# Optimization experiments

Hardware: AMD Instinct MI355X
Metric: run time of the kernel (lower is better)

Reference implementation:

```python
import jax, jax.numpy as jnp
import numpy as np

BN_EPS = 1e-5

def conv1x1(x, w, b):
    # x: [N,C,T,V], w: [O,C], b: [O]
    return jnp.einsum('nctv,oc->notv', x, w) + b[None, :, None, None]

def conv9(x, w, b):
    # (9,1) temporal conv, padding (4,0). x: [N,C,T,V], w: [O,C,9], b: [O]
    out = jax.lax.conv_general_dilated(
        x, w[:, :, :, None], window_strides=(1, 1), padding=((4, 4), (0, 0)),
        dimension_numbers=('NCHW', 'OIHW', 'NCHW'))
    return out + b[None, :, None, None]

def attn_adj(f1, f2):
    # f1,f2: [N,inter,T,V] -> softmax over rows (axis -2) of [N,V,V]
    N, ic, T, V = f1.shape
    a1 = jnp.transpose(f1, (0, 3, 1, 2)).reshape(N, V, ic * T)  # permute(0,3,1,2).view
    a2 = f2.reshape(N, ic * T, V)
    scores = jnp.einsum('nvk,nkw->nvw', a1, a2) / (ic * T)
    return jax.nn.softmax(scores, axis=-2)


def setup_inputs() -> dict:
    key = jax.random.key(0)
    ks = jax.random.split(key, 16)
    N, C, T, V, S, IC = 16, 256, 64, 25, 3, 64
    s = lambda k, shape, sc=0.05: jax.random.normal(k, shape, dtype=jnp.float32) * sc
    return {
        'x': jax.random.normal(ks[0], (N, C, T, V), dtype=jnp.float32),
        'A': jax.random.uniform(ks[1], (S, V, V), dtype=jnp.float32),
        'PA': s(ks[2], (S, V, V), 1e-3),
        'wa': s(ks[3], (S, IC, C)), 'ba': jnp.zeros((S, IC), jnp.float32),
        'wb': s(ks[4], (S, IC, C)), 'bb': jnp.zeros((S, IC), jnp.float32),
        'wT1': s(ks[5], (S, IC, C, 9)), 'bT1': jnp.zeros((S, IC), jnp.float32),
        'wT2': s(ks[6], (S, IC, C, 9)), 'bT2': jnp.zeros((S, IC), jnp.float32),
        'wST11': s(ks[7], (S, IC, C, 9)), 'bST11': jnp.zeros((S, IC), jnp.float32),
        'wST12': s(ks[8], (S, IC, C, 9)), 'bST12': jnp.zeros((S, IC), jnp.float32),
        'wd': s(ks[9], (S, C, C)), 'bd': jnp.zeros((S, C), jnp.float32),
        'gamma': jnp.ones((C,), jnp.float32), 'beta': jnp.zeros((C,), jnp.float32),
        'bn_mean': jnp.zeros((C,), jnp.float32), 'bn_var': jnp.ones((C,), jnp.float32),
    }


def reference(x, A, PA, wa, ba, wb, bb, wT1, bT1, wT2, bT2,
              wST11, bST11, wST12, bST12, wd, bd, gamma, beta, bn_mean, bn_var):
    N, C, T, V = x.shape
    I = jnp.eye(V, dtype=x.dtype)
    # Chebyshev-like static graph transforms (computed once in __init__ in torch)
    A_ch4s = jax.nn.softmax((8 * A**4 - 4 * A**2 - 4 * A + I) / V, axis=-2)
    A_ch3 = 4 * A**2 - A - 2 * I
    A_all = A_ch3 + A_ch4s + PA  # [3,V,V]

    xf = x.reshape(N, C * T, V)
    y = 0.0
    for i in range(3):
        A1 = attn_adj(conv1x1(x, wa[i], ba[i]), conv1x1(x, wb[i], bb[i]))
        AT = attn_adj(conv9(x, wT1[i], bT1[i]), conv9(x, wT2[i], bT2[i]))
        # ModuleList append quirk: even i -> 1x1 conv (center tap), odd i -> (9,1) conv
        if i % 2 == 0:
            s1 = conv1x1(x, wST11[i, :, :, 4], bST11[i])
            s2 = conv1x1(x, wST12[i, :, :, 4], bST12[i])
        else:
            s1 = conv9(x, wST11[i], bST11[i])
            s2 = conv9(x, wST12[i], bST12[i])
        AST = attn_adj(s1, s2)
        Ai = A_all[i] + A1 + AT + AST  # [N,V,V]
        z = jnp.einsum('nkv,nvw->nkw', xf, Ai).reshape(N, C, T, V)
        y = y + conv1x1(z, wd[i], bd[i])

    yb = (y - bn_mean[None, :, None, None]) * (gamma[None, :, None, None]
         / jnp.sqrt(bn_var[None, :, None, None] + BN_EPS)) + beta[None, :, None, None]
    return jax.nn.relu(yb + x)  # down is identity (in_channels == out_channels)
```

## Files before the change

### kernel.cpp

```cpp
#include <hip/hip_runtime.h>
#include <hip/hip_bf16.h>

#define NN 16
#define CC 256
#define TT 64
#define VV 25
#define ICC 64
#define TV 1600
#define CTV 409600
#define NICTV 1638400

typedef __bf16 v8bf __attribute__((ext_vector_type(8)));
typedef __bf16 v4bf __attribute__((ext_vector_type(4)));
typedef float f32x16 __attribute__((ext_vector_type(16)));

struct ConvPairs {
  const __bf16* wA[5];
  const __bf16* wB[5];
  const float*  bA[5];
  const float*  bB[5];
};

__device__ __forceinline__ void gl_lds16(const __bf16* g, __bf16* l){
  __builtin_amdgcn_global_load_lds(
      (const __attribute__((address_space(1))) unsigned int*)g,
      (__attribute__((address_space(3))) unsigned int*)l, 16, 0, 0);
}

__global__ __launch_bounds__(256) void prep_k(
    const float* __restrict__ x, __bf16* __restrict__ xt,
    const float* __restrict__ wT1, const float* __restrict__ wT2,
    const float* __restrict__ wST11, const float* __restrict__ wST12,
    __bf16* __restrict__ wT1p, __bf16* __restrict__ wT2p,
    __bf16* __restrict__ wS1p, __bf16* __restrict__ wS2p,
    const float* __restrict__ wa, const float* __restrict__ wb,
    __bf16* __restrict__ wabp, __bf16* __restrict__ wScp,
    const float* __restrict__ wd, __bf16* __restrict__ wdb,
    const float* __restrict__ A, const float* __restrict__ PA,
    float* __restrict__ Aall, __bf16* __restrict__ zp){
  __shared__ __align__(16) float smf[64*65];
  __bf16* smb = (__bf16*)smf;
  int b = blockIdx.x;
  int tid = threadIdx.x;
  if (b < 64){
    int t = b >> 3, ch64 = (b >> 1) & 3, o2 = b & 1;
    const float* src; __bf16* dst;
    if (t < 3)      { src = wT1  + (size_t)t*147456;     dst = wT1p + (size_t)t*147456; }
    else if (t < 6) { src = wT2  + (size_t)(t-3)*147456; dst = wT2p + (size_t)(t-3)*147456; }
    else if (t == 6){ src = wST11 + 147456;              dst = wS1p; }
    else            { src = wST12 + 147456;              dst = wS2p; }
    const float* in = src + (size_t)(o2*32)*2304 + ch64*576;
    for (int i = tid; i < 32*576; i += 256){
      int row = i / 576, cc = i % 576;
      smb[i] = (__bf16)in[(size_t)row*2304 + cc];
    }
    __syncthreads();
    for (int i = tid; i < 18432; i += 256){
      int e = i & 7, l = (i >> 3) & 63, ks = (i >> 9) & 1;
      int r10 = i >> 10;
      int tap = r10 % 9, chh = r10 / 9;
      int ol = l & 31, hh = l >> 5;
      int cl = ks*16 + hh*8 + e;
      int c64 = chh*32 + cl;
      int ch8 = ch64*2 + chh;
      dst[(size_t)((((ch8*9 + tap)*2 + ks)*2 + o2)*512) + l*8 + e]
          = smb[ol*576 + c64*9 + tap];
    }
  } else if (b < 74){
    int u = b - 64;
    for (int it = 0; it < 8; ++it){
      int i = tid + it*256;
      int e = i & 7, l = (i >> 3) & 63, o2 = (i >> 9) & 1;
      int ks = (i >> 10) & 1, ch = i >> 11;
      int ol = l & 31, hh = l >> 5;
      int o = o2*32 + ol;
      int c = ch*32 + ks*16 + hh*8 + e;
      __bf16 v;
      if (u < 6){
        const float* w = (u < 3) ? (wa + (size_t)u*16384) : (wb + (size_t)(u-3)*16384);
        v = (__bf16)w[(size_t)o*256 + c];
      } else {
        int i9 = ((u == 6) || (u == 8)) ? 0 : 2;
        const float* w = ((u < 8) ? wST11 : wST12) + (size_t)i9*147456;
        v = (__bf16)w[((size_t)o*256 + c)*9 + 4];
      }
      __bf16* dst = (u < 6) ? (wabp + (size_t)u*16384) : (wScp + (size_t)(u-6)*16384);
      dst[i] = v;
    }
  } else if (b < 842){
    int i = (b-74)*256 + tid;
    if (i < 196608) wdb[i] = (__bf16)wd[i];
  } else if (b == 842){
    int t = tid;
    if (t < 75){
      int s = t / 25, w = t % 25;
      float a[25], m[25];
      float mx = -3.4e38f;
      for (int v = 0; v < 25; ++v){
        float av = A[(s*25 + v)*25 + w];
        a[v] = av;
        float d = (v == w) ? 1.f : 0.f;
        float mm = (8.f*av*av*av*av - 4.f*av*av - 4.f*av + d) * 0.04f;
        m[v] = mm;
        mx = fmaxf(mx, mm);
      }
      float sum = 0.f;
      for (int v = 0; v < 25; ++v){ float e = __expf(m[v]-mx); m[v] = e; sum += e; }
      float inv = 1.f/sum;
      for (int v = 0; v < 25; ++v){
        float av = a[v];
        float d = (v == w) ? 1.f : 0.f;
        Aall[(s*25+v)*25 + w] = m[v]*inv + 4.f*av*av - av - 2.f*d + PA[(s*25+v)*25+w];
      }
    } else if (t >= 128){
      zp[t-128] = (__bf16)0.f;
    }
  } else {
    int idx = b - 843;
    int p0 = (idx % 25)*64, c0 = ((idx/25) & 3)*64, n = idx/100;
    for (int i = tid; i < 4096; i += 256){
      int cc = i >> 6, pp = i & 63;
      smf[cc*65+pp] = x[(size_t)n*CTV + (size_t)(c0+cc)*TV + p0 + pp];
    }
    __syncthreads();
    for (int i = tid; i < 4096; i += 256){
      int pp = i >> 6, cc = i & 63;
      xt[((size_t)n*TV + p0+pp)*256 + c0+cc] = (__bf16)smf[cc*65+pp];
    }
  }
}

template<int NTAPS>
__global__ __launch_bounds__(512, 4) void conv14_k(const __bf16* __restrict__ xt,
    ConvPairs cp, const __bf16* __restrict__ zp, __bf16* __restrict__ fbuf){
  extern __shared__ __bf16 sm[];
  constexpr int HALO  = (NTAPS==9) ? 100 : 0;
  constexpr int NROWS = 256 + 2*HALO;
  constexpr int SLOTS = NROWS*4;
  constexpr int KSTG  = (SLOTS + 511)/512;
  constexpr int NSTEP = NTAPS*2;
  int p0 = blockIdx.x*256;
  int n  = blockIdx.y;
  int pr = blockIdx.z;
  int tid = threadIdx.x;
  int lane = tid & 63;
  int wave = tid >> 6;
  int which = wave >> 2, wq = wave & 3;
  int h = lane >> 5, l31 = lane & 31;
  const __bf16* wp = (which ? cp.wB[pr] : cp.wA[pr]) + lane*8;
  const __bf16* xtn = xt + (size_t)n*CTV;
  __bf16* buf0 = sm;
  __bf16* buf1 = sm + NROWS*32;

  f32x16 acc[2][2];
  #pragma unroll
  for (int a=0;a<2;++a)
    #pragma unroll
    for (int b=0;b<2;++b)
      #pragma unroll
      for (int r=0;r<16;++r) acc[a][b][r] = 0.f;

  int rowbase = wq*64 + l31;

  auto stage = [&](__bf16* bn, int ch){
    #pragma unroll
    for (int k=0; k<KSTG; ++k){
      int slot = k*512 + tid;
      if ((SLOTS & 511) && slot >= SLOTS) continue;
      const __bf16* src;
      if (NTAPS == 1){
        int l31s = slot & 31, f = slot >> 5;
        int h_ = f & 1, ks_ = (f >> 1) & 1, pblk = f >> 2;
        int pg = p0 + pblk*32 + l31s;
        src = (pg < 1600) ? (xtn + (size_t)pg*256 + ch*32 + ks_*16 + h_*8)
                          : zp;
      } else {
        int row = slot >> 2, g2 = slot & 3;
        int g = (g2 - (row>>1)) & 3;
        int pg = p0 - HALO + row;
        src = ((unsigned)pg < 1600u) ? (xtn + (size_t)pg*256 + ch*32 + g*8)
                                     : zp;
      }
      gl_lds16(src, bn + (size_t)slot*8);
    }
  };
  auto ldA = [&](int ch, int s, v8bf* aa){
    int tap = s >> 1, ks = s & 1;
    size_t o = (size_t)(((ch*NTAPS + tap)*2 + ks)*2)*512;
    aa[0] = *(const v8bf*)(wp + o);
    aa[1] = *(const v8bf*)(wp + o + 512);
  };
  auto ldB = [&](const __bf16* bc, int s, v8bf* bb){
    int tap = s >> 1, ks = s & 1;
    #pragma unroll
    for (int pq=0; pq<2; ++pq){
      if (NTAPS == 1){
        int frag = ((wq*2 + pq)*2 + ks)*2 + h;
        bb[pq] = *(const v8bf*)(bc + frag*256 + l31*8);
      } else {
        int row = tap*25 + rowbase + pq*32;
        int gs = ((ks*2 + h) + (row>>1)) & 3;
        bb[pq] = *(const v8bf*)(bc + row*32 + gs*8);
      }
    }
  };

  v8bf ar[2][2];
  ldA(0, 0, ar[0]);
  ldA(0, 1, ar[1]);
  stage(buf0, 0);
  __syncthreads();

  for (int ch=0; ch<8; ++ch){
    const __bf16* bc = (ch & 1) ? buf1 : buf0;
    __bf16*       bn = (ch & 1) ? buf0 : buf1;
    if (ch < 7) stage(bn, ch+1);
    v8bf bR[2][2];
    ldB(bc, 0, bR[0]);
    if (NSTEP > 1) ldB(bc, 1, bR[1]);
    #pragma unroll
    for (int s=0; s<NSTEP; ++s){
      int c = s & 1;
      v8bf A0 = ar[c][0], A1 = ar[c][1];
      v8bf B0 = bR[c][0], B1 = bR[c][1];
      if (s+2 < NSTEP){
        ldB(bc, s+2, bR[c]);
        ldA(ch, s+2, ar[c]);
      } else if (ch < 7){
        ldA(ch+1, s+2-NSTEP, ar[c]);
      }
      acc[0][0] = __builtin_amdgcn_mfma_f32_32x32x16_bf16(A0, B0, acc[0][0], 0,0,0);
      acc[1][0] = __builtin_amdgcn_mfma_f32_32x32x16_bf16(A1, B0, acc[1][0], 0,0,0);
      acc[0][1] = __builtin_amdgcn_mfma_f32_32x32x16_bf16(A0, B1, acc[0][1], 0,0,0);
      acc[1][1] = __builtin_amdgcn_mfma_f32_32x32x16_bf16(A1, B1, acc[1][1], 0,0,0);
    }
    __syncthreads();
  }

  const float* bias = which ? cp.bB[pr] : cp.bA[pr];
  __bf16* outb = fbuf + (size_t)(pr*2 + which)*NICTV + (size_t)n*TV*64;
  #pragma unroll
  for (int pq=0; pq<2; ++pq){
    int p = p0 + wq*64 + pq*32 + l31;
    if (p >= 1600) continue;
    __bf16* orow = outb + (size_t)p*64;
    #pragma unroll
    for (int of=0; of<2; ++of){
      #pragma unroll
      for (int g=0; g<4; ++g){
        int og = of*32 + 8*g + 4*h;
        v4bf pk;
        #pragma unroll
        for (int j=0;j<4;++j) pk[j] = (__bf16)(acc[of][pq][4*g+j] + bias[og+j]);
        *(v4bf*)(orow + og) = pk;
      }
    }
  }
}

__global__ __launch_bounds__(256, 2) void ugemm6_k(const __bf16* __restrict__ xt,
    const __bf16* __restrict__ wdb, __bf16* __restrict__ ubuf){
  __shared__ __bf16 sm[64*256];
  int p0 = blockIdx.x*64;
  int n  = blockIdx.y;
  int tid = threadIdx.x;
  int lane = tid & 63;
  int os = tid >> 6;
  int h = lane >> 5, l31 = lane & 31;
  const __bf16* xtn = xt + (size_t)n*CTV;

  for (int s2 = tid; s2 < 64*32; s2 += 256){
    int row = s2 >> 5, g = s2 & 31;
    uint4 val = *(const uint4*)(xtn + (size_t)(p0+row)*256 + g*8);
    int gs = (g + row) & 31;
    *(uint4*)(sm + row*256 + gs*8) = val;
  }
  __syncthreads();

  auto ldB = [&](int ks, v8bf* bb){
    #pragma unroll
    for (int pq=0; pq<2; ++pq){
      int row = pq*32 + l31;
      int gs = ((ks*2 + h) + row) & 31;
      bb[pq] = *(const v8bf*)(sm + row*256 + gs*8);
    }
  };

  for (int br=0; br<3; ++br){
    const __bf16* wl = wdb + ((size_t)br*256 + os*64 + l31)*256 + h*8;
    auto ldA = [&](int ks, v8bf& A0, v8bf& A1){
      A0 = *(const v8bf*)(wl + ks*16);
      A1 = *(const v8bf*)(wl + (size_t)32*256 + ks*16);
    };
    f32x16 acc[2][2];
    #pragma unroll
    for (int a=0;a<2;++a)
      #pragma unroll
      for (int b=0;b<2;++b)
        #pragma unroll
        for (int r=0;r<16;++r) acc[a][b][r] = 0.f;

    v8bf a0[4], a1[4];
    ldA(0, a0[0], a1[0]);
    ldA(1, a0[1], a1[1]);
    ldA(2, a0[2], a1[2]);
    ldA(3, a0[3], a1[3]);
    v8bf bR[2][2];
    ldB(0, bR[0]);
    ldB(1, bR[1]);
    #pragma unroll
    for (int ks=0; ks<16; ++ks){
      int c2 = ks & 1, cur = ks & 3;
      v8bf B0 = bR[c2][0], B1 = bR[c2][1];
      v8bf A0 = a0[cur], A1 = a1[cur];
      if (ks+2 < 16) ldB(ks+2, bR[c2]);
      if (ks+4 < 16) ldA(ks+4, a0[cur], a1[cur]);
      acc[0][0] = __builtin_amdgcn_mfma_f32_32x32x16_bf16(A0, B0, acc[0][0], 0,0,0);
      acc[1][0] = __builtin_amdgcn_mfma_f32_32x32x16_bf16(A1, B0, acc[1][0], 0,0,0);
      acc[0][1] = __builtin_amdgcn_mfma_f32_32x32x16_bf16(A0, B1, acc[0][1], 0,0,0);
      acc[1][1] = __builtin_amdgcn_mfma_f32_32x32x16_bf16(A1, B1, acc[1][1], 0,0,0);
    }

    #pragma unroll
    for (int pq=0; pq<2; ++pq){
      int p = p0 + pq*32 + l31;
      __bf16* out = ubuf + ((size_t)(br*NN + n)*TV + p)*256;
      #pragma unroll
      for (int oq=0; oq<2; ++oq){
        #pragma unroll
        for (int g=0; g<4; ++g){
          int og = os*64 + oq*32 + 8*g + 4*h;
          v4bf pk;
          #pragma unroll
          for (int j=0;j<4;++j) pk[j] = (__bf16)acc[oq][pq][4*g+j];
          *(v4bf*)(out + og) = pk;
        }
      }
    }
  }
}

__global__ __launch_bounds__(256) void scores_m_k(const __bf16* __restrict__ fbuf,
                                                  float* __restrict__ part, int pairbase){
  int n = blockIdx.y, pr = blockIdx.z;
  int tid = threadIdx.x;
  int lane = tid & 63;
  int wave = tid >> 6;
  int chunk = blockIdx.x*4 + wave;
  int h = lane >> 5, l31 = lane & 31;
  const __bf16* f1 = fbuf + (size_t)(pr*2)*NICTV   + (size_t)n*TV*64;
  const __bf16* f2 = fbuf + (size_t)(pr*2+1)*NICTV + (size_t)n*TV*64;
  int t0 = chunk*4;

  f32x16 acc;
  #pragma unroll
  for (int r=0;r<16;++r) acc[r] = 0.f;

  auto off = [&](int s)->size_t{
    int t = t0 + (s>>2), og = s&3;
    return ((size_t)(t*25 + l31))*64 + og*16 + h*8;
  };
  v8bf A[4], B[4];
  #pragma unroll
  for (int i=0; i<4; ++i){
    size_t o = off(i);
    A[i] = *(const v8bf*)(f1+o); B[i] = *(const v8bf*)(f2+o);
  }
  #pragma unroll
  for (int s=0; s<16; ++s){
    int cur = s & 3;
    v8bf Ac = A[cur], Bc = B[cur];
    if (s+4 < 16){
      size_t o2 = off(s+4);
      A[cur] = *(const v8bf*)(f1+o2);
      B[cur] = *(const v8bf*)(f2+o2);
    }
    acc = __builtin_amdgcn_mfma_f32_32x32x16_bf16(Ac, Bc, acc, 0,0,0);
  }

  size_t tile = (((size_t)(pairbase+pr)*NN + n)*16 + chunk);
  float* pt = part + tile*1024;
  #pragma unroll
  for (int r=0; r<16; ++r){
    int row = (r&3) + 8*(r>>2) + 4*h;
    pt[row*32 + l31] = acc[r];
  }
}

__global__ __launch_bounds__(64) void reduce_all_k(const float* __restrict__ part,
    const float* __restrict__ Aall, float* __restrict__ Ai3){
  const int pairbr[9] = {0,1,2,0,2, 0,1,2,1};
  int n = blockIdx.x, w = blockIdx.y;
  int lane = threadIdx.x;
  float accbr[3] = {0.f, 0.f, 0.f};
  for (int pr=0; pr<9; ++pr){
    float s = 0.f;
    if (lane < 25){
      const float* pp = part + (((size_t)pr*NN + n)*16)*1024 + lane*32 + w;
      #pragma unroll
      for (int ch=0; ch<16; ++ch) s += pp[(size_t)ch*1024];
    }
    s *= (1.f/4096.f);
    float mval = (lane<25) ? s : -3.4e38f;
    #pragma unroll
    for (int d=32; d>0; d>>=1) mval = fmaxf(mval, __shfl_xor(mval, d));
    float e = (lane<25) ? __expf(s - mval) : 0.f;
    float sum = e;
    #pragma unroll
    for (int d=32; d>0; d>>=1) sum += __shfl_xor(sum, d);
    accbr[pairbr[pr]] += e / sum;
  }
  if (lane < 25){
    #pragma unroll
    for (int br=0; br<3; ++br)
      Ai3[((size_t)br*NN + n)*625 + lane*25 + w] =
        Aall[br*625 + lane*25 + w] + accbr[br];
  }
}

__global__ __launch_bounds__(256) void yep_k(const float* __restrict__ x,
    const float* __restrict__ Ai3, const __bf16* __restrict__ ubuf,
    const float* __restrict__ bd, const float* __restrict__ gamma,
    const float* __restrict__ beta, const float* __restrict__ bnm,
    const float* __restrict__ bnv, float* __restrict__ out){
  __shared__ float ais[3][25*28];
  int t = blockIdx.x, n = blockIdx.y, o = threadIdx.x;
  for (int l=o; l<2100; l+=256){
    int br = l/700, r = l%700;
    int v = r/28, w = r%28;
    ais[br][v*28+w] = (w<25) ? Ai3[((size_t)br*NN + n)*625 + v*25 + w] : 0.f;
  }
  __syncthreads();
  float y[28];
  #pragma unroll
  for (int w=0;w<28;++w) y[w]=0.f;
  for (int br=0; br<3; ++br){
    const __bf16* up = ubuf + ((size_t)(br*NN + n)*TV + t*25)*256 + o;
    float uv[25];
    #pragma unroll
    for (int v=0;v<25;++v) uv[v] = (float)up[(size_t)v*256];
    const float* ab = ais[br];
    for (int v=0; v<25; ++v){
      float u = uv[v];
      #pragma unroll
      for (int j=0; j<7; ++j){
        float4 a4 = *(const float4*)(ab + v*28 + 4*j);
        y[4*j+0] = fmaf(u, a4.x, y[4*j+0]);
        y[4*j+1] = fmaf(u, a4.y, y[4*j+1]);
        y[4*j+2] = fmaf(u, a4.z, y[4*j+2]);
        y[4*j+3] = fmaf(u, a4.w, y[4*j+3]);
      }
    }
  }
  float bsum = bd[o] + bd[256+o] + bd[512+o];
  float sc = gamma[o] * rsqrtf(bnv[o] + 1e-5f);
  float m  = bnm[o], be = beta[o];
  const float* xr = x + (size_t)n*CTV + (size_t)o*TV + t*25;
  float* orow = out + (size_t)n*CTV + (size_t)o*TV + t*25;
  #pragma unroll
  for (int w=0; w<25; ++w)
    orow[w] = fmaxf((y[w] + bsum - m)*sc + be + xr[w], 0.f);
}

extern "C" void kernel_launch(void* const* d_in, const int* in_sizes, int n_in,
                              void* d_out, int out_size, void* d_ws, size_t ws_size,
                              hipStream_t stream) {
  const float* x     = (const float*)d_in[0];
  const float* A     = (const float*)d_in[1];
  const float* PA    = (const float*)d_in[2];
  const float* wa    = (const float*)d_in[3];
  const float* ba    = (const float*)d_in[4];
  const float* wb    = (const float*)d_in[5];
  const float* bb    = (const float*)d_in[6];
  const float* wT1   = (const float*)d_in[7];
  const float* bT1   = (const float*)d_in[8];
  const float* wT2   = (const float*)d_in[9];
  const float* bT2   = (const float*)d_in[10];
  const float* wST11 = (const float*)d_in[11];
  const float* bST11 = (const float*)d_in[12];
  const float* wST12 = (const float*)d_in[13];
  const float* bST12 = (const float*)d_in[14];
  const float* wd    = (const float*)d_in[15];
  const float* bd    = (const float*)d_in[16];
  const float* gamma = (const float*)d_in[17];
  const float* beta  = (const float*)d_in[18];
  const float* bnm   = (const float*)d_in[19];
  const float* bnv   = (const float*)d_in[20];

  char* W = (char*)d_ws;
  float*  Aall = (float*)W;  W += 8192;
  __bf16* zp   = (__bf16*)W; W += 256;
  float*  Ai3  = (float*)W;  W += 122880;
  __bf16* wabp = (__bf16*)W; W += 196608;
  __bf16* wScp = (__bf16*)W; W += 131072;
  __bf16* wT1p = (__bf16*)W; W += 884736;
  __bf16* wT2p = (__bf16*)W; W += 884736;
  __bf16* wS1p = (__bf16*)W; W += 294912;
  __bf16* wS2p = (__bf16*)W; W += 294912;
  __bf16* wdb  = (__bf16*)W; W += 393216;
  __bf16* xt   = (__bf16*)W; W += 13107200;
  char* R = W;               W += 39321600;
  float*  part = (float*)W;  W += 9437184;
  __bf16* fbuf = (__bf16*)R;
  __bf16* ubuf = (__bf16*)R;

  prep_k<<<2443, 256, 0, stream>>>(x, xt, wT1, wT2, wST11, wST12,
                                   wT1p, wT2p, wS1p, wS2p,
                                   wa, wb, wabp, wScp, wd, wdb, A, PA, Aall, zp);

  {
    ConvPairs cp;
    for (int i=0;i<3;++i){
      cp.wA[i] = wabp + (size_t)i*16384;      cp.wB[i] = wabp + (size_t)(3+i)*16384;
      cp.bA[i] = ba + i*64;                   cp.bB[i] = bb + i*64;
    }
    int evens[2] = {0, 2};
    for (int j=0;j<2;++j){
      int i = evens[j];
      cp.wA[3+j] = wScp + (size_t)j*16384;    cp.wB[3+j] = wScp + (size_t)(2+j)*16384;
      cp.bA[3+j] = bST11 + i*64;              cp.bB[3+j] = bST12 + i*64;
    }
    conv14_k<1><<<dim3(7,16,5), 512, 2*256*32*2, stream>>>(xt, cp, zp, fbuf);
    scores_m_k<<<dim3(4,16,5), 256, 0, stream>>>(fbuf, part, 0);
  }

  {
    ConvPairs cp;
    for (int i=0;i<3;++i){
      cp.wA[i] = wT1p + (size_t)i*147456;  cp.wB[i] = wT2p + (size_t)i*147456;
      cp.bA[i] = bT1 + i*64;               cp.bB[i] = bT2 + i*64;
    }
    cp.wA[3] = wS1p;  cp.wB[3] = wS2p;
    cp.bA[3] = bST11 + 64;  cp.bB[3] = bST12 + 64;
    cp.wA[4] = cp.wA[3]; cp.wB[4] = cp.wB[3]; cp.bA[4] = cp.bA[3]; cp.bB[4] = cp.bB[3];
    conv14_k<9><<<dim3(7,16,4), 512, 2*456*32*2, stream>>>(xt, cp, zp, fbuf);
    scores_m_k<<<dim3(4,16,4), 256, 0, stream>>>(fbuf, part, 5);
  }

  ugemm6_k<<<dim3(25,16), 256, 0, stream>>>(xt, wdb, ubuf);
  reduce_all_k<<<dim3(16,25), 64, 0, stream>>>(part, Aall, Ai3);
  yep_k<<<dim3(64,16), 256, 0, stream>>>(x, Ai3, ubuf, bd, gamma, beta, bnm, bnv,
                                         (float*)d_out);
}
```

Before: 338.4 us.

## Stage conv weights through LDS and deepen MFMA operand prefetch

The conv kernel now copies each channel chunk's weight slices for both conv branches into shared memory with async global-to-LDS loads, instead of having every wave read weights directly from global memory. Operand prefetch depth for the 9-tap variant goes from 2 to 3, and MFMA issue is wrapped in s_setprio. The goal is to cut redundant global weight traffic and hide load latency. In exchange, the 9-tap kernel uses far more shared memory (about 132 KB), which lowers occupancy (min waves per EU reduced to 2), and it adds an extra barrier per chunk because weight staging is not double-buffered.

```diff
diff --git a/kernel.cpp b/kernel.cpp
--- a/kernel.cpp
+++ b/kernel.cpp
@@ -130,8 +130,8 @@
   }
 }
 
-template<int NTAPS>
-__global__ __launch_bounds__(512, 4) void conv14_k(const __bf16* __restrict__ xt,
+template<int NTAPS, int MINW>
+__global__ __launch_bounds__(512, MINW) void conv15_k(const __bf16* __restrict__ xt,
     ConvPairs cp, const __bf16* __restrict__ zp, __bf16* __restrict__ fbuf){
   extern __shared__ __bf16 sm[];
   constexpr int HALO  = (NTAPS==9) ? 100 : 0;
@@ -139,6 +139,9 @@
   constexpr int SLOTS = NROWS*4;
   constexpr int KSTG  = (SLOTS + 511)/512;
   constexpr int NSTEP = NTAPS*2;
+  constexpr int AELE  = NTAPS*2*2*512;
+  constexpr int ASLT  = 2*AELE/8;
+  constexpr int DEP   = (NSTEP >= 3) ? 3 : 2;
   int p0 = blockIdx.x*256;
   int n  = blockIdx.y;
   int pr = blockIdx.z;
@@ -147,10 +150,12 @@
   int wave = tid >> 6;
   int which = wave >> 2, wq = wave & 3;
   int h = lane >> 5, l31 = lane & 31;
-  const __bf16* wp = (which ? cp.wB[pr] : cp.wA[pr]) + lane*8;
   const __bf16* xtn = xt + (size_t)n*CTV;
-  __bf16* buf0 = sm;
-  __bf16* buf1 = sm + NROWS*32;
+  const __bf16* wg0 = cp.wA[pr];
+  const __bf16* wg1 = cp.wB[pr];
+  __bf16* xb0 = sm;
+  __bf16* xb1 = sm + NROWS*32;
+  __bf16* Ab  = sm + 2*NROWS*32;
 
   f32x16 acc[2][2];
   #pragma unroll
@@ -162,7 +167,7 @@
 
   int rowbase = wq*64 + l31;
 
-  auto stage = [&](__bf16* bn, int ch){
+  auto stageX = [&](__bf16* bn, int ch){
     #pragma unroll
     for (int k=0; k<KSTG; ++k){
       int slot = k*512 + tid;
@@ -184,11 +189,22 @@
       gl_lds16(src, bn + (size_t)slot*8);
     }
   };
-  auto ldA = [&](int ch, int s, v8bf* aa){
-    int tap = s >> 1, ks = s & 1;
-    size_t o = (size_t)(((ch*NTAPS + tap)*2 + ks)*2)*512;
-    aa[0] = *(const v8bf*)(wp + o);
-    aa[1] = *(const v8bf*)(wp + o + 512);
+  auto stageA = [&](int ch){
+    #pragma unroll
+    for (int k=0; k<(ASLT+511)/512; ++k){
+      int slot = k*512 + tid;
+      if ((ASLT & 511) && slot >= ASLT) continue;
+      int cv = (slot >= AELE/8) ? 1 : 0;
+      int off = (slot - cv*(AELE/8))*8;
+      const __bf16* src = (cv ? wg1 : wg0) + (size_t)ch*AELE + off;
+      gl_lds16(src, Ab + cv*AELE + off);
+    }
+  };
+  const __bf16* aw = Ab + which*AELE + lane*8;
+  auto ldA = [&](int s, v8bf* aa){
+    int off = s*1024;
+    aa[0] = *(const v8bf*)(aw + off);
+    aa[1] = *(const v8bf*)(aw + off + 512);
   };
   auto ldB = [&](const __bf16* bc, int s, v8bf* bb){
     int tap = s >> 1, ks = s & 1;
@@ -205,35 +221,37 @@
     }
   };
 
-  v8bf ar[2][2];
-  ldA(0, 0, ar[0]);
-  ldA(0, 1, ar[1]);
-  stage(buf0, 0);
+  stageA(0);
+  stageX(xb0, 0);
   __syncthreads();
 
+  v8bf ar[DEP][2], bR[DEP][2];
   for (int ch=0; ch<8; ++ch){
-    const __bf16* bc = (ch & 1) ? buf1 : buf0;
-    __bf16*       bn = (ch & 1) ? buf0 : buf1;
-    if (ch < 7) stage(bn, ch+1);
-    v8bf bR[2][2];
-    ldB(bc, 0, bR[0]);
-    if (NSTEP > 1) ldB(bc, 1, bR[1]);
+    const __bf16* bc = (ch & 1) ? xb1 : xb0;
+    __bf16*       bn = (ch & 1) ? xb0 : xb1;
+    if (ch < 7) stageX(bn, ch+1);
+    #pragma unroll
+    for (int i=0; i<DEP; ++i){
+      if (i < NSTEP){ ldA(i, ar[i]); ldB(bc, i, bR[i]); }
+    }
     #pragma unroll
     for (int s=0; s<NSTEP; ++s){
-      int c = s & 1;
+      int c = s % DEP;
       v8bf A0 = ar[c][0], A1 = ar[c][1];
       v8bf B0 = bR[c][0], B1 = bR[c][1];
-      if (s+2 < NSTEP){
-        ldB(bc, s+2, bR[c]);
-        ldA(ch, s+2, ar[c]);
-      } else if (ch < 7){
-        ldA(ch+1, s+2-NSTEP, ar[c]);
-      }
+      if (s+DEP < NSTEP){
+        ldB(bc, s+DEP, bR[c]);
+        ldA(s+DEP, ar[c]);
+      }
+      __builtin_amdgcn_s_setprio(1);
       acc[0][0] = __builtin_amdgcn_mfma_f32_32x32x16_bf16(A0, B0, acc[0][0], 0,0,0);
       acc[1][0] = __builtin_amdgcn_mfma_f32_32x32x16_bf16(A1, B0, acc[1][0], 0,0,0);
       acc[0][1] = __builtin_amdgcn_mfma_f32_32x32x16_bf16(A0, B1, acc[0][1], 0,0,0);
       acc[1][1] = __builtin_amdgcn_mfma_f32_32x32x16_bf16(A1, B1, acc[1][1], 0,0,0);
-    }
+      __builtin_amdgcn_s_setprio(0);
+    }
+    __syncthreads();
+    if (ch < 7) stageA(ch+1);
     __syncthreads();
   }
 
@@ -520,7 +538,7 @@
       cp.wA[3+j] = wScp + (size_t)j*16384;    cp.wB[3+j] = wScp + (size_t)(2+j)*16384;
       cp.bA[3+j] = bST11 + i*64;              cp.bB[3+j] = bST12 + i*64;
     }
-    conv14_k<1><<<dim3(7,16,5), 512, 2*256*32*2, stream>>>(xt, cp, zp, fbuf);
+    conv15_k<1,4><<<dim3(7,16,5), 512, 40960, stream>>>(xt, cp, zp, fbuf);
     scores_m_k<<<dim3(4,16,5), 256, 0, stream>>>(fbuf, part, 0);
   }
 
@@ -533,7 +551,7 @@
     cp.wA[3] = wS1p;  cp.wB[3] = wS2p;
     cp.bA[3] = bST11 + 64;  cp.bB[3] = bST12 + 64;
     cp.wA[4] = cp.wA[3]; cp.wB[4] = cp.wB[3]; cp.bA[4] = cp.bA[3]; cp.bB[4] = cp.bB[3];
-    conv14_k<9><<<dim3(7,16,4), 512, 2*456*32*2, stream>>>(xt, cp, zp, fbuf);
+    conv15_k<9,2><<<dim3(7,16,4), 512, 132096, stream>>>(xt, cp, zp, fbuf);
     scores_m_k<<<dim3(4,16,4), 256, 0, stream>>>(fbuf, part, 5);
   }
 
```

Result: faster. 328.4 us (-3.0%).
